# Kernel optimization log

Measured on AMD Instinct MI355X. Metric: run time of the kernel, lower is better.

## Reference

```python
import jax, jax.numpy as jnp
import numpy as np


def setup_inputs() -> dict:
    key = jax.random.key(0)
    k1, k2, k3 = jax.random.split(key, 3)
    B, H, I, O, Dp1 = 4, 2048, 1024, 1024, 4  # degree=3 -> degree+1=4
    x = jax.random.normal(k1, (B, H, I, Dp1), dtype=jnp.float32)
    weight = 0.1 * jax.random.normal(k2, (O, Dp1), dtype=jnp.float32)
    weighted_sum = 0.1 * jax.random.normal(k3, (O, I), dtype=jnp.float32)
    return {"x": x, "weight": weight, "weighted_sum": weighted_sum}


def reference(x, weight, weighted_sum):
    # Original: weights[o,i,d] = weighted_sum[o,i] * weight[o,d];
    #           out[b,h,o] = sum_{i,d} x[b,h,i,d] * weights[o,i,d]
    # Fused 3-operand einsum avoids materializing the (O, I, D+1) intermediate.
    return jnp.einsum('bhid,oi,od->bho', x, weighted_sum, weight)
```

## Files before the change

### kernel.cpp

```cpp
#include <hip/hip_runtime.h>

typedef unsigned short u16;
typedef u16 u16x4 __attribute__((ext_vector_type(4)));
typedef float f32x4 __attribute__((ext_vector_type(4)));
typedef __bf16 bf16x8 __attribute__((ext_vector_type(8)));
typedef __bf16 bf16x4 __attribute__((ext_vector_type(4)));

#define M_DIM 8192
#define N_DIM 1024
#define K_DIM 4096

__device__ __forceinline__ u16 f2bf(float f) {
  unsigned u = __float_as_uint(f);
  u += 0x7FFFu + ((u >> 16) & 1u);
  return (u16)(u >> 16);
}

__global__ __launch_bounds__(256) void k_w2(const float* __restrict__ w,
                                            const float* __restrict__ ws,
                                            u16* __restrict__ w2) {
  int idx = blockIdx.x * 256 + threadIdx.x;
  int o = idx >> 10;
  float s = ws[idx];
  f32x4 wv = *(const f32x4*)(w + o * 4);
  u16x4 r;
  r[0] = f2bf(s * wv[0]); r[1] = f2bf(s * wv[1]);
  r[2] = f2bf(s * wv[2]); r[3] = f2bf(s * wv[3]);
  *(u16x4*)(w2 + (size_t)idx * 4) = r;
}

typedef __attribute__((address_space(1))) const void gvoid_t;
typedef __attribute__((address_space(3))) void lvoid_t;
__device__ __forceinline__ void gll16(const void* g, void* l) {
  __builtin_amdgcn_global_load_lds((gvoid_t*)g, (lvoid_t*)l, 16, 0, 0);
}

__device__ __forceinline__ void cvt_store(u16* dst, f32x4 a) {
  bf16x4 b;
  b[0] = (__bf16)a[0]; b[1] = (__bf16)a[1];
  b[2] = (__bf16)a[2]; b[3] = (__bf16)a[3];
  *(bf16x4*)dst = b;
}

__global__ __launch_bounds__(512) void k_gemm(const float* __restrict__ A,
                                              const u16* __restrict__ Bt,
                                              float* __restrict__ C) {
  __shared__ u16 sA[128 * 64];
  __shared__ u16 sB[128 * 64];

  const int t    = threadIdx.x;
  const int lane = t & 63;
  const int wid  = t >> 6;

  const int L  = blockIdx.x;
  const int xc = L & 7;
  const int jj = L >> 3;
  const int m0 = (xc * 8 + (jj >> 3)) * 128;
  const int n0 = (jj & 7) * 128;

  const int ar  = t >> 4;
  const int aq  = t & 15;
  const int apc = (aq >> 1) ^ (ar & 7);
  const float* pA = A + (size_t)(m0 + ar) * K_DIM + aq * 4;
  u16* lA = sA + ar * 64 + apc * 8 + (aq & 1) * 4;

  const int s0 = t, s1 = t + 512;
  const int r0 = s0 >> 3, c0 = (s0 & 7) ^ (r0 & 7);
  const int r1 = s1 >> 3, c1 = (s1 & 7) ^ (r1 & 7);
  const u16* gB0 = Bt + (size_t)(n0 + r0) * K_DIM + c0 * 8;
  const u16* gB1 = Bt + (size_t)(n0 + r1) * K_DIM + c1 * 8;
  u16* lB0 = sB + s0 * 8;  u16* lB1 = sB + s1 * 8;

  const int wm = (wid >> 1) * 32;
  const int wn = (wid & 1) * 64;
  const int fr = lane & 15;
  const int lc = lane >> 4;

  f32x4 acc[2][4];
#pragma unroll
  for (int i = 0; i < 2; i++)
#pragma unroll
    for (int j = 0; j < 4; j++) acc[i][j] = (f32x4){0.f, 0.f, 0.f, 0.f};

  f32x4 pf0 = *(const f32x4*)(pA);
  f32x4 pf1 = *(const f32x4*)(pA + (size_t)32 * K_DIM);
  f32x4 pf2 = *(const f32x4*)(pA + (size_t)64 * K_DIM);
  f32x4 pf3 = *(const f32x4*)(pA + (size_t)96 * K_DIM);

  for (int k0 = 0; k0 < K_DIM; k0 += 64) {
    cvt_store(lA,           pf0);
    cvt_store(lA + 32 * 64, pf1);
    cvt_store(lA + 64 * 64, pf2);
    cvt_store(lA + 96 * 64, pf3);
    gll16(gB0, lB0); gll16(gB1, lB1);
    gB0 += 64; gB1 += 64;
    __syncthreads();

    if (k0 + 64 < K_DIM) {
      pA += 64;
      pf0 = *(const f32x4*)(pA);
      pf1 = *(const f32x4*)(pA + (size_t)32 * K_DIM);
      pf2 = *(const f32x4*)(pA + (size_t)64 * K_DIM);
      pf3 = *(const f32x4*)(pA + (size_t)96 * K_DIM);
    }

#pragma unroll
    for (int ks = 0; ks < 2; ks++) {
      bf16x8 af[2], bfr[4];
#pragma unroll
      for (int mi = 0; mi < 2; mi++) {
        int r  = wm + mi * 16 + fr;
        int pc = (ks * 4 + lc) ^ (r & 7);
        af[mi] = *(const bf16x8*)(sA + r * 64 + pc * 8);
      }
#pragma unroll
      for (int ni = 0; ni < 4; ni++) {
        int r  = wn + ni * 16 + fr;
        int pc = (ks * 4 + lc) ^ (r & 7);
        bfr[ni] = *(const bf16x8*)(sB + r * 64 + pc * 8);
      }
#pragma unroll
      for (int mi = 0; mi < 2; mi++)
#pragma unroll
        for (int ni = 0; ni < 4; ni++)
          acc[mi][ni] = __builtin_amdgcn_mfma_f32_16x16x32_bf16(
              af[mi], bfr[ni], acc[mi][ni], 0, 0, 0);
    }
    __syncthreads();
  }

  const int cr = (lane >> 4) * 4;
  const int cc = lane & 15;
#pragma unroll
  for (int mi = 0; mi < 2; mi++)
#pragma unroll
    for (int ni = 0; ni < 4; ni++) {
      float* cp = C + (size_t)(m0 + wm + mi * 16 + cr) * N_DIM +
                  (n0 + wn + ni * 16 + cc);
#pragma unroll
      for (int r = 0; r < 4; r++) cp[(size_t)r * N_DIM] = acc[mi][ni][r];
    }
}

extern "C" void kernel_launch(void* const* d_in, const int* in_sizes, int n_in,
                              void* d_out, int out_size, void* d_ws, size_t ws_size,
                              hipStream_t stream) {
  const float* x  = (const float*)d_in[0];
  const float* w  = (const float*)d_in[1];
  const float* ws = (const float*)d_in[2];
  float* out = (float*)d_out;

  u16* w2 = (u16*)d_ws;

  k_w2<<<4096, 256, 0, stream>>>(w, ws, w2);
  k_gemm<<<512, 512, 0, stream>>>(x, w2, out);
}
```

Before: 271.8 us.

## Double-buffer LDS tiles to overlap global loads with MFMA compute

Splits the A and B shared-memory tiles into two buffers. The next B tile is loaded asynchronously via global_load_lds and the next A tile is written after compute, so only one barrier per K-step is needed instead of two. This is meant to hide global load latency behind the MFMA work. LDS use doubles to 64KB per block, which may reduce occupancy.

```diff
diff --git a/kernel.cpp b/kernel.cpp
--- a/kernel.cpp
+++ b/kernel.cpp
@@ -45,8 +45,8 @@
 __global__ __launch_bounds__(512) void k_gemm(const float* __restrict__ A,
                                               const u16* __restrict__ Bt,
                                               float* __restrict__ C) {
-  __shared__ u16 sA[128 * 64];
-  __shared__ u16 sB[128 * 64];
+  __shared__ u16 sA[2][128 * 64];
+  __shared__ u16 sB[2][128 * 64];
 
   const int t    = threadIdx.x;
   const int lane = t & 63;
@@ -62,14 +62,14 @@
   const int aq  = t & 15;
   const int apc = (aq >> 1) ^ (ar & 7);
   const float* pA = A + (size_t)(m0 + ar) * K_DIM + aq * 4;
-  u16* lA = sA + ar * 64 + apc * 8 + (aq & 1) * 4;
+  const int lAoff = ar * 64 + apc * 8 + (aq & 1) * 4;
 
   const int s0 = t, s1 = t + 512;
   const int r0 = s0 >> 3, c0 = (s0 & 7) ^ (r0 & 7);
   const int r1 = s1 >> 3, c1 = (s1 & 7) ^ (r1 & 7);
   const u16* gB0 = Bt + (size_t)(n0 + r0) * K_DIM + c0 * 8;
   const u16* gB1 = Bt + (size_t)(n0 + r1) * K_DIM + c1 * 8;
-  u16* lB0 = sB + s0 * 8;  u16* lB1 = sB + s1 * 8;
+  const int lB0off = s0 * 8, lB1off = s1 * 8;
 
   const int wm = (wid >> 1) * 32;
   const int wn = (wid & 1) * 64;
@@ -86,22 +86,27 @@
   f32x4 pf1 = *(const f32x4*)(pA + (size_t)32 * K_DIM);
   f32x4 pf2 = *(const f32x4*)(pA + (size_t)64 * K_DIM);
   f32x4 pf3 = *(const f32x4*)(pA + (size_t)96 * K_DIM);
+  gll16(gB0, sB[0] + lB0off); gll16(gB1, sB[0] + lB1off);
+  gB0 += 64; gB1 += 64;
+  cvt_store(sA[0] + lAoff,           pf0);
+  cvt_store(sA[0] + lAoff + 32 * 64, pf1);
+  cvt_store(sA[0] + lAoff + 64 * 64, pf2);
+  cvt_store(sA[0] + lAoff + 96 * 64, pf3);
+  __syncthreads();
 
   for (int k0 = 0; k0 < K_DIM; k0 += 64) {
-    cvt_store(lA,           pf0);
-    cvt_store(lA + 32 * 64, pf1);
-    cvt_store(lA + 64 * 64, pf2);
-    cvt_store(lA + 96 * 64, pf3);
-    gll16(gB0, lB0); gll16(gB1, lB1);
-    gB0 += 64; gB1 += 64;
-    __syncthreads();
+    const int cur = (k0 >> 6) & 1;
+    const int nxt = cur ^ 1;
+    const bool has_next = (k0 + 64 < K_DIM);
 
-    if (k0 + 64 < K_DIM) {
+    if (has_next) {
       pA += 64;
       pf0 = *(const f32x4*)(pA);
       pf1 = *(const f32x4*)(pA + (size_t)32 * K_DIM);
       pf2 = *(const f32x4*)(pA + (size_t)64 * K_DIM);
       pf3 = *(const f32x4*)(pA + (size_t)96 * K_DIM);
+      gll16(gB0, sB[nxt] + lB0off); gll16(gB1, sB[nxt] + lB1off);
+      gB0 += 64; gB1 += 64;
     }
 
 #pragma unroll
@@ -111,13 +116,13 @@
       for (int mi = 0; mi < 2; mi++) {
         int r  = wm + mi * 16 + fr;
         int pc = (ks * 4 + lc) ^ (r & 7);
-        af[mi] = *(const bf16x8*)(sA + r * 64 + pc * 8);
+        af[mi] = *(const bf16x8*)(sA[cur] + r * 64 + pc * 8);
       }
 #pragma unroll
       for (int ni = 0; ni < 4; ni++) {
         int r  = wn + ni * 16 + fr;
         int pc = (ks * 4 + lc) ^ (r & 7);
-        bfr[ni] = *(const bf16x8*)(sB + r * 64 + pc * 8);
+        bfr[ni] = *(const bf16x8*)(sB[cur] + r * 64 + pc * 8);
       }
 #pragma unroll
       for (int mi = 0; mi < 2; mi++)
@@ -126,7 +131,14 @@
           acc[mi][ni] = __builtin_amdgcn_mfma_f32_16x16x32_bf16(
               af[mi], bfr[ni], acc[mi][ni], 0, 0, 0);
     }
-    __syncthreads();
+
+    if (has_next) {
+      cvt_store(sA[nxt] + lAoff,           pf0);
+      cvt_store(sA[nxt] + lAoff + 32 * 64, pf1);
+      cvt_store(sA[nxt] + lAoff + 64 * 64, pf2);
+      cvt_store(sA[nxt] + lAoff + 96 * 64, pf3);
+      __syncthreads();
+    }
   }
 
   const int cr = (lane >> 4) * 4;
```

Result: slower. 293.0 us (+7.8%).

## Double-buffer LDS with two-deep register prefetch in GEMM main loop

Applied to the files above, without the earlier changes.

Replaces the single-buffered loop, which used two barriers per K-step, with ping-pong LDS buffers and two register sets of prefetched global data, leaving one barrier per step. B is now loaded through registers rather than direct global-to-LDS loads, so B's global loads are issued two steps ahead alongside A's. This is meant to hide global-load latency and halve synchronisation. In exchange it doubles LDS use to 64 KB per block and adds register pressure from two prefetch sets, with a launch-bounds occupancy hint that may not be attainable.

```diff
diff --git a/kernel.cpp b/kernel.cpp
--- a/kernel.cpp
+++ b/kernel.cpp
@@ -2,6 +2,7 @@
 
 typedef unsigned short u16;
 typedef u16 u16x4 __attribute__((ext_vector_type(4)));
+typedef u16 u16x8 __attribute__((ext_vector_type(8)));
 typedef float f32x4 __attribute__((ext_vector_type(4)));
 typedef __bf16 bf16x8 __attribute__((ext_vector_type(8)));
 typedef __bf16 bf16x4 __attribute__((ext_vector_type(4)));
@@ -29,11 +30,6 @@
   *(u16x4*)(w2 + (size_t)idx * 4) = r;
 }
 
-typedef __attribute__((address_space(1))) const void gvoid_t;
-typedef __attribute__((address_space(3))) void lvoid_t;
-__device__ __forceinline__ void gll16(const void* g, void* l) {
-  __builtin_amdgcn_global_load_lds((gvoid_t*)g, (lvoid_t*)l, 16, 0, 0);
-}
 
 __device__ __forceinline__ void cvt_store(u16* dst, f32x4 a) {
   bf16x4 b;
@@ -42,11 +38,21 @@
   *(bf16x4*)dst = b;
 }
 
-__global__ __launch_bounds__(512) void k_gemm(const float* __restrict__ A,
-                                              const u16* __restrict__ Bt,
-                                              float* __restrict__ C) {
-  __shared__ u16 sA[128 * 64];
-  __shared__ u16 sB[128 * 64];
+__device__ __forceinline__ void lds_barrier() {
+  asm volatile("s_waitcnt lgkmcnt(0)" ::: "memory");
+  __builtin_amdgcn_s_barrier();
+}
+
+struct Set {
+  f32x4 a0, a1, a2, a3;
+  u16x8 b0, b1;
+};
+
+__global__ __launch_bounds__(512, 4) void k_gemm(const float* __restrict__ A,
+                                                 const u16* __restrict__ Bt,
+                                                 float* __restrict__ C) {
+  __shared__ u16 sA[2][128 * 64];
+  __shared__ u16 sB[2][128 * 64];
 
   const int t    = threadIdx.x;
   const int lane = t & 63;
@@ -62,14 +68,14 @@
   const int aq  = t & 15;
   const int apc = (aq >> 1) ^ (ar & 7);
   const float* pA = A + (size_t)(m0 + ar) * K_DIM + aq * 4;
-  u16* lA = sA + ar * 64 + apc * 8 + (aq & 1) * 4;
+  const int lAoff = ar * 64 + apc * 8 + (aq & 1) * 4;
 
   const int s0 = t, s1 = t + 512;
   const int r0 = s0 >> 3, c0 = (s0 & 7) ^ (r0 & 7);
   const int r1 = s1 >> 3, c1 = (s1 & 7) ^ (r1 & 7);
   const u16* gB0 = Bt + (size_t)(n0 + r0) * K_DIM + c0 * 8;
   const u16* gB1 = Bt + (size_t)(n0 + r1) * K_DIM + c1 * 8;
-  u16* lB0 = sB + s0 * 8;  u16* lB1 = sB + s1 * 8;
+  const int lB0off = s0 * 8, lB1off = s1 * 8;
 
   const int wm = (wid >> 1) * 32;
   const int wn = (wid & 1) * 64;
@@ -82,52 +88,79 @@
 #pragma unroll
     for (int j = 0; j < 4; j++) acc[i][j] = (f32x4){0.f, 0.f, 0.f, 0.f};
 
-  f32x4 pf0 = *(const f32x4*)(pA);
-  f32x4 pf1 = *(const f32x4*)(pA + (size_t)32 * K_DIM);
-  f32x4 pf2 = *(const f32x4*)(pA + (size_t)64 * K_DIM);
-  f32x4 pf3 = *(const f32x4*)(pA + (size_t)96 * K_DIM);
+#define LOAD_SET(S)                                   \
+  do {                                                \
+    S.a0 = *(const f32x4*)(pA);                       \
+    S.a1 = *(const f32x4*)(pA + (size_t)32 * K_DIM);  \
+    S.a2 = *(const f32x4*)(pA + (size_t)64 * K_DIM);  \
+    S.a3 = *(const f32x4*)(pA + (size_t)96 * K_DIM);  \
+    S.b0 = *(const u16x8*)(gB0);                      \
+    S.b1 = *(const u16x8*)(gB1);                      \
+    pA += 64; gB0 += 64; gB1 += 64;                   \
+  } while (0)
 
-  for (int k0 = 0; k0 < K_DIM; k0 += 64) {
-    cvt_store(lA,           pf0);
-    cvt_store(lA + 32 * 64, pf1);
-    cvt_store(lA + 64 * 64, pf2);
-    cvt_store(lA + 96 * 64, pf3);
-    gll16(gB0, lB0); gll16(gB1, lB1);
-    gB0 += 64; gB1 += 64;
-    __syncthreads();
+#define WRITE_SET(S, bufA, bufB)                      \
+  do {                                                \
+    cvt_store((bufA) + lAoff,           S.a0);        \
+    cvt_store((bufA) + lAoff + 32 * 64, S.a1);        \
+    cvt_store((bufA) + lAoff + 64 * 64, S.a2);        \
+    cvt_store((bufA) + lAoff + 96 * 64, S.a3);        \
+    *(u16x8*)((bufB) + lB0off) = S.b0;                \
+    *(u16x8*)((bufB) + lB1off) = S.b1;                \
+  } while (0)
 
-    if (k0 + 64 < K_DIM) {
-      pA += 64;
-      pf0 = *(const f32x4*)(pA);
-      pf1 = *(const f32x4*)(pA + (size_t)32 * K_DIM);
-      pf2 = *(const f32x4*)(pA + (size_t)64 * K_DIM);
-      pf3 = *(const f32x4*)(pA + (size_t)96 * K_DIM);
-    }
+#define COMPUTE(bufA, bufB)                                          \
+  do {                                                               \
+    _Pragma("unroll")                                                \
+    for (int ks = 0; ks < 2; ks++) {                                 \
+      bf16x8 af[2], bfr[4];                                          \
+      _Pragma("unroll")                                              \
+      for (int mi = 0; mi < 2; mi++) {                               \
+        int r  = wm + mi * 16 + fr;                                  \
+        int pc = (ks * 4 + lc) ^ (r & 7);                            \
+        af[mi] = *(const bf16x8*)((bufA) + r * 64 + pc * 8);         \
+      }                                                              \
+      _Pragma("unroll")                                              \
+      for (int ni = 0; ni < 4; ni++) {                               \
+        int r  = wn + ni * 16 + fr;                                  \
+        int pc = (ks * 4 + lc) ^ (r & 7);                            \
+        bfr[ni] = *(const bf16x8*)((bufB) + r * 64 + pc * 8);        \
+      }                                                              \
+      _Pragma("unroll")                                              \
+      for (int mi = 0; mi < 2; mi++)                                 \
+        _Pragma("unroll")                                            \
+        for (int ni = 0; ni < 4; ni++)                               \
+          acc[mi][ni] = __builtin_amdgcn_mfma_f32_16x16x32_bf16(     \
+              af[mi], bfr[ni], acc[mi][ni], 0, 0, 0);                \
+    }                                                                \
+  } while (0)
 
-#pragma unroll
-    for (int ks = 0; ks < 2; ks++) {
-      bf16x8 af[2], bfr[4];
-#pragma unroll
-      for (int mi = 0; mi < 2; mi++) {
-        int r  = wm + mi * 16 + fr;
-        int pc = (ks * 4 + lc) ^ (r & 7);
-        af[mi] = *(const bf16x8*)(sA + r * 64 + pc * 8);
-      }
-#pragma unroll
-      for (int ni = 0; ni < 4; ni++) {
-        int r  = wn + ni * 16 + fr;
-        int pc = (ks * 4 + lc) ^ (r & 7);
-        bfr[ni] = *(const bf16x8*)(sB + r * 64 + pc * 8);
-      }
-#pragma unroll
-      for (int mi = 0; mi < 2; mi++)
-#pragma unroll
-        for (int ni = 0; ni < 4; ni++)
-          acc[mi][ni] = __builtin_amdgcn_mfma_f32_16x16x32_bf16(
-              af[mi], bfr[ni], acc[mi][ni], 0, 0, 0);
-    }
-    __syncthreads();
+  Set S0, S1;
+
+  LOAD_SET(S0);
+  LOAD_SET(S1);
+  WRITE_SET(S0, sA[0], sB[0]);
+  lds_barrier();
+
+  for (int j = 0; j < 31; ++j) {
+    LOAD_SET(S0);
+    COMPUTE(sA[0], sB[0]);
+    WRITE_SET(S1, sA[1], sB[1]);
+    lds_barrier();
+    LOAD_SET(S1);
+    COMPUTE(sA[1], sB[1]);
+    WRITE_SET(S0, sA[0], sB[0]);
+    lds_barrier();
   }
+
+  COMPUTE(sA[0], sB[0]);
+  WRITE_SET(S1, sA[1], sB[1]);
+  lds_barrier();
+  COMPUTE(sA[1], sB[1]);
+
+#undef LOAD_SET
+#undef WRITE_SET
+#undef COMPUTE
 
   const int cr = (lane >> 4) * 4;
   const int cc = lane & 15;
```

Result: slower. 290.7 us (+7.0%).
